# Optimization experiments

Measured on AMD Instinct MI355X. Metric: run time of the kernel, lower is better.

The kernel has to match this reference:

```python
import jax, jax.numpy as jnp
import numpy as np

E = 6        # num_experts
C = 256      # embed_dim (expert in_channels)
HID = 256    # mlp_dim (expert hidden_channels)
META = 9
GATE_H = 128
BN_EPS = 1e-5  # torch BatchNorm2d default


def _conv(x, w):
    # x: [1,Cin,H,W], w: [Cout,Cin,3,3] -> [1,Cout,H,W], padding=1
    return jax.lax.conv_general_dilated(
        x, w, window_strides=(1, 1), padding=((1, 1), (1, 1)),
        dimension_numbers=("NCHW", "OIHW", "NCHW"))


def _bn(x, mean, var, gamma, beta):
    # inference-mode BatchNorm2d over channel dim
    scale = gamma * jax.lax.rsqrt(var + BN_EPS)
    return (x - mean[None, :, None, None]) * scale[None, :, None, None] + beta[None, :, None, None]


def setup_inputs() -> dict:
    key = jax.random.key(0)
    ks = jax.random.split(key, 20)
    B, H, W = 16, 64, 64
    f32 = jnp.float32
    return {
        "moe_c4": jax.random.normal(ks[0], (B, C, H, W), f32),
        "meta": jax.random.normal(ks[1], (B, META), f32),
        # Gate MLP: Linear(9,128) -> ReLU -> Linear(128,6)
        "gate_w1": jax.random.normal(ks[2], (META, GATE_H), f32) * 0.3,
        "gate_b1": jnp.zeros((GATE_H,), f32),
        "gate_w2": jax.random.normal(ks[3], (GATE_H, E), f32) * 0.1,
        "gate_b2": jnp.zeros((E,), f32),
        # Expert conv1: Conv2d(C, HID, 3) + BN(HID), stacked over experts
        "conv1_w": jax.random.normal(ks[4], (E, HID, C, 3, 3), f32) * 0.02,
        "conv1_b": jnp.zeros((E, HID), f32),
        "bn1_g": jnp.ones((E, HID), f32) + 0.1 * jax.random.normal(ks[5], (E, HID), f32),
        "bn1_b": 0.1 * jax.random.normal(ks[6], (E, HID), f32),
        "bn1_m": 0.1 * jax.random.normal(ks[7], (E, HID), f32),
        "bn1_v": jax.random.uniform(ks[8], (E, HID), f32) + 0.5,
        # Expert conv2: Conv2d(HID, C, 3) + BN(C)
        "conv2_w": jax.random.normal(ks[9], (E, C, HID, 3, 3), f32) * 0.02,
        "conv2_b": jnp.zeros((E, C), f32),
        "bn2_g": jnp.ones((E, C), f32) + 0.1 * jax.random.normal(ks[10], (E, C), f32),
        "bn2_b": 0.1 * jax.random.normal(ks[11], (E, C), f32),
        "bn2_m": 0.1 * jax.random.normal(ks[12], (E, C), f32),
        "bn2_v": jax.random.uniform(ks[13], (E, C), f32) + 0.5,
    }


def reference(moe_c4, meta, gate_w1, gate_b1, gate_w2, gate_b2,
              conv1_w, conv1_b, bn1_g, bn1_b, bn1_m, bn1_v,
              conv2_w, conv2_b, bn2_g, bn2_b, bn2_m, bn2_v):
    # --- Gate: MLP -> softmax -> top-1 routing ---
    h = jax.nn.relu(meta @ gate_w1 + gate_b1)
    gate_probs = jax.nn.softmax(h @ gate_w2 + gate_b2, axis=-1)  # [B,E]
    top1 = jnp.argmax(gate_probs, axis=-1)                        # [B]

    # --- Dispatch: gather each sample's expert params, run one conv stack per sample ---
    def one(x, w1, b1, g1, be1, m1, v1, w2, b2, g2, be2, m2, v2):
        y = _conv(x[None], w1) + b1[None, :, None, None]
        y = jax.nn.relu(_bn(y, m1, v1, g1, be1))
        y = _conv(y, w2) + b2[None, :, None, None]
        y = jax.nn.relu(_bn(y, m2, v2, g2, be2))
        return y[0]

    out = jax.vmap(one)(
        moe_c4,
        conv1_w[top1], conv1_b[top1], bn1_g[top1], bn1_b[top1], bn1_m[top1], bn1_v[top1],
        conv2_w[top1], conv2_b[top1], bn2_g[top1], bn2_b[top1], bn2_m[top1], bn2_v[top1])

    # --- Load-balance loss (torch.std is unbiased -> ddof=1) ---
    importance = gate_probs.sum(axis=0) / (gate_probs.sum() + 1e-8)
    balance_loss = jnp.std(importance, ddof=1)
    return out, balance_loss
```

## Files before the change

kernel.cpp:

```cpp
#include <hip/hip_runtime.h>
#include <hip/hip_bf16.h>

typedef unsigned short u16;
typedef unsigned int u32;
typedef __attribute__((ext_vector_type(8))) short short8_v;
typedef __attribute__((ext_vector_type(4))) float float4_v;

__device__ __forceinline__ u16 f2bf(float f) {
  u32 u = __float_as_uint(f);
  return (u16)((u + 0x7fffu + ((u >> 16) & 1u)) >> 16);
}

__device__ __forceinline__ void gl_lds16(const void* g, void* l) {
  __builtin_amdgcn_global_load_lds(
      (const __attribute__((address_space(1))) u32*)g,
      (__attribute__((address_space(3))) u32*)l, 16, 0, 0);
}

__global__ void gate_kernel(const float* __restrict__ meta,
                            const float* __restrict__ gw1, const float* __restrict__ gb1,
                            const float* __restrict__ gw2, const float* __restrict__ gb2,
                            int* __restrict__ top1, float* __restrict__ loss_out) {
  const int tid = threadIdx.x;
  __shared__ float logits[16][6];
  __shared__ float red[2][6];
  __shared__ float probs[16][6];
  float w2c[6];
  #pragma unroll
  for (int k = 0; k < 6; ++k) w2c[k] = gw2[tid * 6 + k];
  const float b1v = gb1[tid];
  for (int b = 0; b < 16; ++b) {
    float h = b1v;
    #pragma unroll
    for (int i = 0; i < 9; ++i) h += meta[b * 9 + i] * gw1[i * 128 + tid];
    h = fmaxf(h, 0.f);
    float v[6];
    #pragma unroll
    for (int k = 0; k < 6; ++k) v[k] = h * w2c[k];
    #pragma unroll
    for (int off = 32; off >= 1; off >>= 1)
      #pragma unroll
      for (int k = 0; k < 6; ++k) v[k] += __shfl_down(v[k], off, 64);
    if ((tid & 63) == 0)
      for (int k = 0; k < 6; ++k) red[tid >> 6][k] = v[k];
    __syncthreads();
    if (tid < 6) logits[b][tid] = red[0][tid] + red[1][tid] + gb2[tid];
    __syncthreads();
  }
  if (tid < 16) {
    const int b = tid;
    float m = logits[b][0];
    for (int k = 1; k < 6; ++k) m = fmaxf(m, logits[b][k]);
    float s = 0.f, p[6];
    for (int k = 0; k < 6; ++k) { p[k] = expf(logits[b][k] - m); s += p[k]; }
    int best = 0; float bm = p[0];
    for (int k = 1; k < 6; ++k) if (p[k] > bm) { bm = p[k]; best = k; }
    top1[b] = best;
    for (int k = 0; k < 6; ++k) probs[b][k] = p[k] / s;
  }
  __syncthreads();
  if (tid == 0) {
    float col[6] = {0, 0, 0, 0, 0, 0}, tot = 0.f;
    for (int b = 0; b < 16; ++b)
      for (int k = 0; k < 6; ++k) col[k] += probs[b][k];
    for (int k = 0; k < 6; ++k) tot += col[k];
    float imp[6], mean = 0.f;
    for (int k = 0; k < 6; ++k) { imp[k] = col[k] / (tot + 1e-8f); mean += imp[k]; }
    mean *= (1.f / 6.f);
    float var = 0.f;
    for (int k = 0; k < 6; ++k) { float d = imp[k] - mean; var += d * d; }
    loss_out[0] = sqrtf(var * 0.2f);
  }
}

__global__ void fold_kernel(const float* c1b, const float* g1, const float* be1, const float* m1, const float* v1,
                            const float* c2b, const float* g2, const float* be2, const float* m2, const float* v2,
                            float* fold1, float* fold2) {
  int t = blockIdx.x * 256 + threadIdx.x;
  if (t >= 3072) return;
  int conv = t / 1536, r = t % 1536;
  if (conv == 0) {
    float scale = g1[r] * rsqrtf(v1[r] + 1e-5f);
    float shift = (c1b[r] - m1[r]) * scale + be1[r];
    fold1[r * 2] = scale; fold1[r * 2 + 1] = shift;
  } else {
    float scale = g2[r] * rsqrtf(v2[r] + 1e-5f);
    float shift = (c2b[r] - m2[r]) * scale + be2[r];
    fold2[r * 2] = scale; fold2[r * 2 + 1] = shift;
  }
}

__global__ void wprep_kernel(const float* __restrict__ w1, const float* __restrict__ w2,
                             u16* __restrict__ w1t, u16* __restrict__ w2t) {
  int t = blockIdx.x * 256 + threadIdx.x;
  const int PER = 442368;
  if (t >= 2 * PER) return;
  const float* wsrc; u16* wdst; int r;
  if (t < PER) { wsrc = w1; wdst = w1t; r = t; }
  else         { wsrc = w2; wdst = w2t; r = t - PER; }
  int e = r / 73728;
  int rem = r % 73728;
  int tap = rem / 8192;
  int rem2 = rem % 8192;
  int co = rem2 >> 5;
  int ci0 = (rem2 & 31) * 8;
  const float* sp = wsrc + (((size_t)e * 256 + co) * 256 + ci0) * 9 + tap;
  u16 v[8];
  #pragma unroll
  for (int j = 0; j < 8; ++j) v[j] = f2bf(sp[j * 9]);
  u32 p0 = v[0] | ((u32)v[1] << 16);
  u32 p1 = v[2] | ((u32)v[3] << 16);
  u32 p2 = v[4] | ((u32)v[5] << 16);
  u32 p3 = v[6] | ((u32)v[7] << 16);
  int4 pk = {(int)p0, (int)p1, (int)p2, (int)p3};
  *(int4*)(wdst + (((size_t)e * 9 + tap) * 256 + co) * 256 + ci0) = pk;
}

__global__ void transpose_pad_kernel(const float* __restrict__ x, u16* __restrict__ xpt) {
  const int b = blockIdx.x >> 6, r = blockIdx.x & 63;
  const int tid = threadIdx.x;
  __shared__ u16 tile[64 * 258];
  const int ci_sub = tid >> 6, c = tid & 63;
  const float* xb = x + ((size_t)b * 256) * 4096 + r * 64 + c;
  for (int k = 0; k < 64; ++k) {
    int ci = k * 4 + ci_sub;
    tile[c * 258 + ci] = f2bf(xb[(size_t)ci * 4096]);
  }
  __syncthreads();
  u16* dstb = xpt + ((size_t)b * 4356 + (size_t)(r + 1) * 66 + 1) * 256;
  #pragma unroll
  for (int it = 0; it < 8; ++it) {
    int chunk = it * 256 + tid;
    int cc = chunk >> 5, part = chunk & 31;
    const u32* lp = (const u32*)(tile + cc * 258 + part * 8);
    int4 vv = {(int)lp[0], (int)lp[1], (int)lp[2], (int)lp[3]};
    *(int4*)(dstb + (size_t)cc * 256 + part * 8) = vv;
  }
}

__global__ void border_zero_kernel(u16* xpt, u16* hpt) {
  int t = blockIdx.x * 256 + threadIdx.x;
  const int TOT = 2 * 16 * 260 * 32;
  if (t >= TOT) return;
  int buf = t / (16 * 260 * 32);
  int r = t % (16 * 260 * 32);
  int b = r / (260 * 32);
  int r2 = r % (260 * 32);
  int idx = r2 >> 5, part = r2 & 31;
  int rc;
  if (idx < 66) rc = idx;
  else if (idx < 132) rc = 65 * 66 + (idx - 66);
  else { int rem = idx - 132; rc = (1 + (rem >> 1)) * 66 + (rem & 1) * 65; }
  u16* base = buf ? hpt : xpt;
  int4 z = {0, 0, 0, 0};
  *(int4*)(base + ((size_t)b * 4356 + rc) * 256 + part * 8) = z;
}

template <int MODE>
__global__ __launch_bounds__(256, 2) void conv_mfma_kernel(
    const u16* __restrict__ src, const u16* __restrict__ wt,
    const int* __restrict__ top1, const float* __restrict__ fold,
    float* __restrict__ outF, u16* __restrict__ outH) {
  __shared__ char Ab[8192];
  __shared__ char Bb[17408];
  const int tid = threadIdx.x;
  const int lane = tid & 63;
  const int wid = tid >> 6;
  const int wr = wid >> 1, wc = wid & 1;
  const int ptile = blockIdx.x, cot = blockIdx.y, b = blockIdx.z;
  const int e = top1[b];

  const char* srcB0 = (const char*)src + ((size_t)b * 4356 + (size_t)ptile * 132) * 512;
  const char* wA0 = (const char*)wt + ((size_t)e * 9 * 65536 + (size_t)cot * 32768) * 2;

  float4_v acc[4][4];
  #pragma unroll
  for (int m = 0; m < 4; ++m)
    #pragma unroll
    for (int n = 0; n < 4; ++n)
      acc[m][n] = (float4_v){0.f, 0.f, 0.f, 0.f};

  for (int chunk = 0; chunk < 8; ++chunk) {
    #pragma unroll
    for (int tap = 0; tap < 9; ++tap) {
      __syncthreads();
      if (tap == 0) {
        const char* sB = srcB0 + chunk * 64;
        const int u0 = wid * 256;
        #pragma unroll
        for (int i = 0; i < 4; ++i) {
          int u = u0 + i * 64 + lane;
          int du = u >> 2;
          int qs = (u & 3) ^ ((u >> 3) & 3);
          gl_lds16(sB + (size_t)du * 512 + qs * 16, Bb + (size_t)(u0 + i * 64) * 16);
        }
        if (wid == 0) {
          int u = 1024 + lane;
          int du = u >> 2;
          int qs = (u & 3) ^ ((u >> 3) & 3);
          gl_lds16(sB + (size_t)du * 512 + qs * 16, Bb + 1024 * 16);
        }
      }
      {
        const char* sA = wA0 + (size_t)tap * 131072 + chunk * 64;
        const int u0 = wid * 128;
        #pragma unroll
        for (int i = 0; i < 2; ++i) {
          int u = u0 + i * 64 + lane;
          int cl = u >> 2;
          int qs = (u & 3) ^ ((u >> 3) & 3);
          gl_lds16(sA + (size_t)cl * 512 + qs * 16, Ab + (size_t)(u0 + i * 64) * 16);
        }
      }
      __syncthreads();

      const int kh = tap / 3, kw = tap % 3;
      short8_v av[4], bv[4];
      #pragma unroll
      for (int m = 0; m < 4; ++m) {
        int cl = wr * 64 + m * 16 + (lane & 15);
        int slot = (lane >> 4) ^ ((cl >> 1) & 3);
        av[m] = *(const short8_v*)(Ab + cl * 64 + slot * 16);
      }
      #pragma unroll
      for (int n = 0; n < 4; ++n) {
        int pt = wc * 64 + n * 16 + (lane & 15);
        int rc = ((pt >> 6) + kh) * 66 + (pt & 63) + kw;
        int slot = (lane >> 4) ^ ((rc >> 1) & 3);
        bv[n] = *(const short8_v*)(Bb + rc * 64 + slot * 16);
      }
      #pragma unroll
      for (int m = 0; m < 4; ++m)
        #pragma unroll
        for (int n = 0; n < 4; ++n)
          acc[m][n] = __builtin_amdgcn_mfma_f32_16x16x32_bf16(av[m], bv[n], acc[m][n], 0, 0, 0);
    }
  }

  const float* fe = fold + (size_t)e * 512;
  #pragma unroll
  for (int m = 0; m < 4; ++m) {
    const int cb = cot * 128 + wr * 64 + m * 16 + ((lane >> 4) << 2);
    float sc0 = fe[(cb + 0) * 2], sh0 = fe[(cb + 0) * 2 + 1];
    float sc1 = fe[(cb + 1) * 2], sh1 = fe[(cb + 1) * 2 + 1];
    float sc2 = fe[(cb + 2) * 2], sh2 = fe[(cb + 2) * 2 + 1];
    float sc3 = fe[(cb + 3) * 2], sh3 = fe[(cb + 3) * 2 + 1];
    #pragma unroll
    for (int n = 0; n < 4; ++n) {
      const int pt = ptile * 128 + wc * 64 + n * 16 + (lane & 15);
      float v0 = fmaxf(acc[m][n][0] * sc0 + sh0, 0.f);
      float v1 = fmaxf(acc[m][n][1] * sc1 + sh1, 0.f);
      float v2 = fmaxf(acc[m][n][2] * sc2 + sh2, 0.f);
      float v3 = fmaxf(acc[m][n][3] * sc3 + sh3, 0.f);
      if (MODE == 1) {
        const size_t rc = (size_t)((pt >> 6) + 1) * 66 + (pt & 63) + 1;
        uint2 pk;
        pk.x = (u32)f2bf(v0) | ((u32)f2bf(v1) << 16);
        pk.y = (u32)f2bf(v2) | ((u32)f2bf(v3) << 16);
        *(uint2*)(outH + ((size_t)b * 4356 + rc) * 256 + cb) = pk;
      } else {
        float* ob = outF + (size_t)b * 1048576;
        ob[(size_t)(cb + 0) * 4096 + pt] = v0;
        ob[(size_t)(cb + 1) * 4096 + pt] = v1;
        ob[(size_t)(cb + 2) * 4096 + pt] = v2;
        ob[(size_t)(cb + 3) * 4096 + pt] = v3;
      }
    }
  }
}

extern "C" void kernel_launch(void* const* d_in, const int* in_sizes, int n_in,
                              void* d_out, int out_size, void* d_ws, size_t ws_size,
                              hipStream_t stream) {
  const float* x    = (const float*)d_in[0];
  const float* meta = (const float*)d_in[1];
  const float* gw1  = (const float*)d_in[2];
  const float* gb1  = (const float*)d_in[3];
  const float* gw2  = (const float*)d_in[4];
  const float* gb2  = (const float*)d_in[5];
  const float* c1w  = (const float*)d_in[6];
  const float* c1b  = (const float*)d_in[7];
  const float* bn1g = (const float*)d_in[8];
  const float* bn1b = (const float*)d_in[9];
  const float* bn1m = (const float*)d_in[10];
  const float* bn1v = (const float*)d_in[11];
  const float* c2w  = (const float*)d_in[12];
  const float* c2b  = (const float*)d_in[13];
  const float* bn2g = (const float*)d_in[14];
  const float* bn2b = (const float*)d_in[15];
  const float* bn2m = (const float*)d_in[16];
  const float* bn2v = (const float*)d_in[17];

  char* ws = (char*)d_ws;
  u16* xpt   = (u16*)(ws);
  u16* hpt   = (u16*)(ws + 35684352);
  u16* w1t   = (u16*)(ws + 71368704);
  u16* w2t   = (u16*)(ws + 78446592);
  float* fold1 = (float*)(ws + 85524480);
  float* fold2 = (float*)(ws + 85536768);
  int* top1  = (int*)(ws + 85549056);

  float* outF = (float*)d_out;
  float* loss = outF + 16777216;

  hipLaunchKernelGGL(gate_kernel, dim3(1), dim3(128), 0, stream,
                     meta, gw1, gb1, gw2, gb2, top1, loss);
  hipLaunchKernelGGL(fold_kernel, dim3(12), dim3(256), 0, stream,
                     c1b, bn1g, bn1b, bn1m, bn1v, c2b, bn2g, bn2b, bn2m, bn2v, fold1, fold2);
  hipLaunchKernelGGL(wprep_kernel, dim3(3456), dim3(256), 0, stream, c1w, c2w, w1t, w2t);
  hipLaunchKernelGGL(transpose_pad_kernel, dim3(1024), dim3(256), 0, stream, x, xpt);
  hipLaunchKernelGGL(border_zero_kernel, dim3(1040), dim3(256), 0, stream, xpt, hpt);
  hipLaunchKernelGGL((conv_mfma_kernel<1>), dim3(32, 2, 16), dim3(256), 0, stream,
                     xpt, w1t, top1, fold1, (float*)nullptr, hpt);
  hipLaunchKernelGGL((conv_mfma_kernel<2>), dim3(32, 2, 16), dim3(256), 0, stream,
                     hpt, w2t, top1, fold2, outF, (u16*)nullptr);
}
```

Baseline: 380.5 us.

## Widen conv tile to all output channels, swizzle grid, coalesce prep kernels

Each conv block now computes all 256 output channels (8x4 MFMA accumulators per wave) rather than splitting channels across two blocks, so the shared input tile is loaded once instead of twice. The launch grid becomes 1D with a swizzle that spreads consecutive blocks across samples. The weight prep kernel stages each output channel's weights in LDS before transposing, and the input transpose reads float4 for coalescing. In exchange each thread holds twice the accumulator registers, which may reduce occupancy or cause spills, and there are half as many blocks.

Measured after the change: 339.8 us. 10.7% less time.

```diff
diff --git a/kernel.cpp b/kernel.cpp
--- a/kernel.cpp
+++ b/kernel.cpp
@@ -92,39 +92,44 @@
 
 __global__ void wprep_kernel(const float* __restrict__ w1, const float* __restrict__ w2,
                              u16* __restrict__ w1t, u16* __restrict__ w2t) {
-  int t = blockIdx.x * 256 + threadIdx.x;
-  const int PER = 442368;
-  if (t >= 2 * PER) return;
-  const float* wsrc; u16* wdst; int r;
-  if (t < PER) { wsrc = w1; wdst = w1t; r = t; }
-  else         { wsrc = w2; wdst = w2t; r = t - PER; }
-  int e = r / 73728;
-  int rem = r % 73728;
-  int tap = rem / 8192;
-  int rem2 = rem % 8192;
-  int co = rem2 >> 5;
-  int ci0 = (rem2 & 31) * 8;
-  const float* sp = wsrc + (((size_t)e * 256 + co) * 256 + ci0) * 9 + tap;
-  u16 v[8];
-  #pragma unroll
-  for (int j = 0; j < 8; ++j) v[j] = f2bf(sp[j * 9]);
-  u32 p0 = v[0] | ((u32)v[1] << 16);
-  u32 p1 = v[2] | ((u32)v[3] << 16);
-  u32 p2 = v[4] | ((u32)v[5] << 16);
-  u32 p3 = v[6] | ((u32)v[7] << 16);
-  int4 pk = {(int)p0, (int)p1, (int)p2, (int)p3};
-  *(int4*)(wdst + (((size_t)e * 9 + tap) * 256 + co) * 256 + ci0) = pk;
+  const int tid = threadIdx.x;
+  const int conv = blockIdx.x >= 1536 ? 1 : 0;
+  const int r = blockIdx.x - (conv ? 1536 : 0);
+  const int e = r >> 8, co = r & 255;
+  const float* src = (conv ? w2 : w1) + (size_t)r * 2304;
+  u16* wdst = conv ? w2t : w1t;
+  __shared__ float buf[2304];
+  const float4* s4 = (const float4*)src;
+  for (int k = tid; k < 576; k += 256) ((float4*)buf)[k] = s4[k];
+  __syncthreads();
+  for (int j = tid; j < 288; j += 256) {
+    int tap = j >> 5, ci0 = (j & 31) * 8;
+    u16 v[8];
+    #pragma unroll
+    for (int i = 0; i < 8; ++i) v[i] = f2bf(buf[(ci0 + i) * 9 + tap]);
+    int4 pk;
+    pk.x = (int)((u32)v[0] | ((u32)v[1] << 16));
+    pk.y = (int)((u32)v[2] | ((u32)v[3] << 16));
+    pk.z = (int)((u32)v[4] | ((u32)v[5] << 16));
+    pk.w = (int)((u32)v[6] | ((u32)v[7] << 16));
+    *(int4*)(wdst + (((size_t)e * 9 + tap) * 256 + co) * 256 + ci0) = pk;
+  }
 }
 
 __global__ void transpose_pad_kernel(const float* __restrict__ x, u16* __restrict__ xpt) {
   const int b = blockIdx.x >> 6, r = blockIdx.x & 63;
   const int tid = threadIdx.x;
   __shared__ u16 tile[64 * 258];
-  const int ci_sub = tid >> 6, c = tid & 63;
-  const float* xb = x + ((size_t)b * 256) * 4096 + r * 64 + c;
-  for (int k = 0; k < 64; ++k) {
-    int ci = k * 4 + ci_sub;
-    tile[c * 258 + ci] = f2bf(xb[(size_t)ci * 4096]);
+  const int cg = tid & 15, ci_g = tid >> 4;
+  const float4* xb4 = (const float4*)(x + ((size_t)b * 256) * 4096 + r * 64);
+  #pragma unroll
+  for (int k = 0; k < 16; ++k) {
+    int ci = k * 16 + ci_g;
+    float4 v = xb4[(size_t)ci * 1024 + cg];
+    tile[(cg * 4 + 0) * 258 + ci] = f2bf(v.x);
+    tile[(cg * 4 + 1) * 258 + ci] = f2bf(v.y);
+    tile[(cg * 4 + 2) * 258 + ci] = f2bf(v.z);
+    tile[(cg * 4 + 3) * 258 + ci] = f2bf(v.w);
   }
   __syncthreads();
   u16* dstb = xpt + ((size_t)b * 4356 + (size_t)(r + 1) * 66 + 1) * 256;
@@ -161,21 +166,23 @@
     const u16* __restrict__ src, const u16* __restrict__ wt,
     const int* __restrict__ top1, const float* __restrict__ fold,
     float* __restrict__ outF, u16* __restrict__ outH) {
-  __shared__ char Ab[8192];
+  __shared__ char Ab[16384];
   __shared__ char Bb[17408];
   const int tid = threadIdx.x;
   const int lane = tid & 63;
   const int wid = tid >> 6;
   const int wr = wid >> 1, wc = wid & 1;
-  const int ptile = blockIdx.x, cot = blockIdx.y, b = blockIdx.z;
+  const int orig = blockIdx.x;
+  const int swz = (orig & 7) * 64 + (orig >> 3);
+  const int ptile = swz & 31, b = swz >> 5;
   const int e = top1[b];
 
   const char* srcB0 = (const char*)src + ((size_t)b * 4356 + (size_t)ptile * 132) * 512;
-  const char* wA0 = (const char*)wt + ((size_t)e * 9 * 65536 + (size_t)cot * 32768) * 2;
-
-  float4_v acc[4][4];
-  #pragma unroll
-  for (int m = 0; m < 4; ++m)
+  const char* wA0 = (const char*)wt + (size_t)e * 9 * 65536 * 2;
+
+  float4_v acc[8][4];
+  #pragma unroll
+  for (int m = 0; m < 8; ++m)
     #pragma unroll
     for (int n = 0; n < 4; ++n)
       acc[m][n] = (float4_v){0.f, 0.f, 0.f, 0.f};
@@ -203,9 +210,9 @@
       }
       {
         const char* sA = wA0 + (size_t)tap * 131072 + chunk * 64;
-        const int u0 = wid * 128;
+        const int u0 = wid * 256;
         #pragma unroll
-        for (int i = 0; i < 2; ++i) {
+        for (int i = 0; i < 4; ++i) {
           int u = u0 + i * 64 + lane;
           int cl = u >> 2;
           int qs = (u & 3) ^ ((u >> 3) & 3);
@@ -215,13 +222,7 @@
       __syncthreads();
 
       const int kh = tap / 3, kw = tap % 3;
-      short8_v av[4], bv[4];
-      #pragma unroll
-      for (int m = 0; m < 4; ++m) {
-        int cl = wr * 64 + m * 16 + (lane & 15);
-        int slot = (lane >> 4) ^ ((cl >> 1) & 3);
-        av[m] = *(const short8_v*)(Ab + cl * 64 + slot * 16);
-      }
+      short8_v bv[4];
       #pragma unroll
       for (int n = 0; n < 4; ++n) {
         int pt = wc * 64 + n * 16 + (lane & 15);
@@ -230,17 +231,21 @@
         bv[n] = *(const short8_v*)(Bb + rc * 64 + slot * 16);
       }
       #pragma unroll
-      for (int m = 0; m < 4; ++m)
+      for (int m = 0; m < 8; ++m) {
+        int cl = wr * 128 + m * 16 + (lane & 15);
+        int slot = (lane >> 4) ^ ((cl >> 1) & 3);
+        short8_v avm = *(const short8_v*)(Ab + cl * 64 + slot * 16);
         #pragma unroll
         for (int n = 0; n < 4; ++n)
-          acc[m][n] = __builtin_amdgcn_mfma_f32_16x16x32_bf16(av[m], bv[n], acc[m][n], 0, 0, 0);
+          acc[m][n] = __builtin_amdgcn_mfma_f32_16x16x32_bf16(avm, bv[n], acc[m][n], 0, 0, 0);
+      }
     }
   }
 
   const float* fe = fold + (size_t)e * 512;
   #pragma unroll
-  for (int m = 0; m < 4; ++m) {
-    const int cb = cot * 128 + wr * 64 + m * 16 + ((lane >> 4) << 2);
+  for (int m = 0; m < 8; ++m) {
+    const int cb = wr * 128 + m * 16 + ((lane >> 4) << 2);
     float sc0 = fe[(cb + 0) * 2], sh0 = fe[(cb + 0) * 2 + 1];
     float sc1 = fe[(cb + 1) * 2], sh1 = fe[(cb + 1) * 2 + 1];
     float sc2 = fe[(cb + 2) * 2], sh2 = fe[(cb + 2) * 2 + 1];
@@ -307,11 +312,11 @@
                      meta, gw1, gb1, gw2, gb2, top1, loss);
   hipLaunchKernelGGL(fold_kernel, dim3(12), dim3(256), 0, stream,
                      c1b, bn1g, bn1b, bn1m, bn1v, c2b, bn2g, bn2b, bn2m, bn2v, fold1, fold2);
-  hipLaunchKernelGGL(wprep_kernel, dim3(3456), dim3(256), 0, stream, c1w, c2w, w1t, w2t);
+  hipLaunchKernelGGL(wprep_kernel, dim3(3072), dim3(256), 0, stream, c1w, c2w, w1t, w2t);
   hipLaunchKernelGGL(transpose_pad_kernel, dim3(1024), dim3(256), 0, stream, x, xpt);
   hipLaunchKernelGGL(border_zero_kernel, dim3(1040), dim3(256), 0, stream, xpt, hpt);
-  hipLaunchKernelGGL((conv_mfma_kernel<1>), dim3(32, 2, 16), dim3(256), 0, stream,
+  hipLaunchKernelGGL((conv_mfma_kernel<1>), dim3(512), dim3(256), 0, stream,
                      xpt, w1t, top1, fold1, (float*)nullptr, hpt);
-  hipLaunchKernelGGL((conv_mfma_kernel<2>), dim3(32, 2, 16), dim3(256), 0, stream,
+  hipLaunchKernelGGL((conv_mfma_kernel<2>), dim3(512), dim3(256), 0, stream,
                      hpt, w2t, top1, fold2, outF, (u16*)nullptr);
 }
```
